# Performance work log

Measured on AMD Instinct MI355X. Metric: run time of the kernel, lower is better.

The kernel has to match this reference:

```python
import jax, jax.numpy as jnp
import numpy as np

B, N_SOURCES, H, W = 32, 262144, 256, 256


def setup_inputs() -> dict:
    key = jax.random.key(0)
    k1, k2, k3, k4 = jax.random.split(key, 4)
    return {
        "point_rates": jax.random.uniform(k1, (B, N_SOURCES), dtype=jnp.float32),
        "spatial": jax.random.uniform(k2, (B, 2, H, W), dtype=jnp.float32),
        "gia": jax.random.uniform(k3, (B, H, W), dtype=jnp.float32),
        "all_source_coords": jax.random.uniform(k4, (N_SOURCES, 2), dtype=jnp.float32),
    }


def reference(point_rates, spatial, gia, all_source_coords):
    # point_rates: [B, N], spatial: [B, 2, H, W], gia: [B, H, W], coords: [N, 2]
    _, _, h, w = spatial.shape
    sx = all_source_coords[:, 0]  # [N]
    sy = all_source_coords[:, 1]  # [N]

    def per_batch(pr, sp, g):
        # pr: [N], sp: [2, H, W], g: [H, W]
        xmin, xmax = sp[0].min(), sp[0].max()
        ymin, ymax = sp[1].min(), sp[1].max()
        in_view = ((sx >= xmin) & (sx <= xmax) & (sy >= ymin) & (sy <= ymax))
        nx = (sx - xmin) / (xmax - xmin)
        ny = (sy - ymin) / (ymax - ymin)
        px = jnp.clip(jnp.round(nx * (w - 1)).astype(jnp.int32), 0, w - 1)
        py = jnp.clip(jnp.round(ny * (h - 1)).astype(jnp.int32), 0, h - 1)
        # out-of-view sources contribute zero (instead of being gathered out)
        em = pr * g[py, px] * in_view.astype(pr.dtype)  # [N]
        field = jnp.zeros((h, w), dtype=pr.dtype).at[py, px].add(em)
        return field[None]  # [1, H, W]

    return jax.vmap(per_batch)(point_rates, spatial, gia)  # [B, 1, H, W]
```

## Files before the change

### kernel.cpp

```cpp
#include <hip/hip_runtime.h>
#include <math.h>

#define BATCH 32
#define NSRC  262144
#define HH    256
#define WW    256
#define HW    (HH * WW)
#define NBLK  16

#define ZBANDS 16
#define ZBAND_PIX (HW / ZBANDS)
#define ZCAP   18432
#define SPILL_CAP 131072
#define FIX_SCALE 524288.0f
#define FIX_INV   (1.0f / 524288.0f)
#define WS_ZCURS_OFF  8192
#define WS_ZSPCNT_OFF 10240
#define WS_ZSPILL_OFF 16384
#define WS_ZARENA_OFF (WS_ZSPILL_OFF + SPILL_CAP * 8)
#define WS_Z_BYTES    (WS_ZARENA_OFF + (size_t)BATCH * ZBANDS * ZCAP * 4)

#define FB_BANDS 8
#define FB_BAND_PIX (HW / FB_BANDS)

__global__ void box_kernel(const float* __restrict__ spatial,
                           float4* __restrict__ partials,
                           unsigned int* __restrict__ zero_tab,
                           int zero_n) {
    const int b   = blockIdx.y;
    const int blk = blockIdx.x;
    const int tid = threadIdx.x;

    if (zero_tab && blk == 0 && b == 0) {
        for (int j = tid; j < zero_n; j += 256) zero_tab[j] = 0u;
    }

    const int chunk = HW / NBLK;
    const float* xs = spatial + (size_t)b * 2 * HW + (size_t)blk * chunk;
    const float* ys = xs + HW;

    float xmn = 1e30f, xmx = -1e30f, ymn = 1e30f, ymx = -1e30f;
    const float4* xs4 = (const float4*)xs;
    const float4* ys4 = (const float4*)ys;
#pragma unroll
    for (int k = 0; k < 4; k++) {
        float4 vx = xs4[k * 256 + tid];
        float4 vy = ys4[k * 256 + tid];
        xmn = fminf(xmn, fminf(fminf(vx.x, vx.y), fminf(vx.z, vx.w)));
        xmx = fmaxf(xmx, fmaxf(fmaxf(vx.x, vx.y), fmaxf(vx.z, vx.w)));
        ymn = fminf(ymn, fminf(fminf(vy.x, vy.y), fminf(vy.z, vy.w)));
        ymx = fmaxf(ymx, fmaxf(fmaxf(vy.x, vy.y), fmaxf(vy.z, vy.w)));
    }
#pragma unroll
    for (int off = 32; off > 0; off >>= 1) {
        xmn = fminf(xmn, __shfl_down(xmn, off));
        xmx = fmaxf(xmx, __shfl_down(xmx, off));
        ymn = fminf(ymn, __shfl_down(ymn, off));
        ymx = fmaxf(ymx, __shfl_down(ymx, off));
    }
    __shared__ float4 s[4];
    if ((tid & 63) == 0) s[tid >> 6] = make_float4(xmn, xmx, ymn, ymx);
    __syncthreads();
    if (tid == 0) {
        float4 r = s[0];
#pragma unroll
        for (int wv = 1; wv < 4; wv++) {
            float4 t = s[wv];
            r.x = fminf(r.x, t.x); r.y = fmaxf(r.y, t.y);
            r.z = fminf(r.z, t.z); r.w = fmaxf(r.w, t.w);
        }
        partials[b * NBLK + blk] = r;
    }
}

__device__ __forceinline__ float4 fold_box(const float4* __restrict__ partials,
                                           int b, int tid, float4* sbox) {
    if (tid < 64) {
        float4 p = make_float4(1e30f, -1e30f, 1e30f, -1e30f);
        if (tid < NBLK) p = partials[b * NBLK + tid];
        float xmn = p.x, xmx = p.y, ymn = p.z, ymx = p.w;
#pragma unroll
        for (int off = 8; off > 0; off >>= 1) {
            xmn = fminf(xmn, __shfl_down(xmn, off));
            xmx = fmaxf(xmx, __shfl_down(xmx, off));
            ymn = fminf(ymn, __shfl_down(ymn, off));
            ymx = fmaxf(ymx, __shfl_down(ymx, off));
        }
        if (tid == 0) *sbox = make_float4(xmn, xmx, ymn, ymx);
    }
    __syncthreads();
    return *sbox;
}

__device__ __forceinline__ int route_of(float cx, float cy, float xmin,
                                        float ymin, float invx, float invy) {
    const float nx = __fmul_rn(__fsub_rn(cx, xmin), invx);
    const float ny = __fmul_rn(__fsub_rn(cy, ymin), invy);
    int px = (int)rintf(__fmul_rn(nx, 255.0f));
    int py = (int)rintf(__fmul_rn(ny, 255.0f));
    px = px < 0 ? 0 : (px > 255 ? 255 : px);
    py = py < 0 ? 0 : (py > 255 ? 255 : py);
    return py * WW + px;
}


__global__ __launch_bounds__(256) void scatter_lds_kernel(
    const float* __restrict__ point_rates, const float2* __restrict__ coords,
    const float4* __restrict__ partials, unsigned int* __restrict__ cursors,
    unsigned int* __restrict__ arena, unsigned int* __restrict__ spill_cnt,
    uint2* __restrict__ spill) {
    const int b   = blockIdx.y;
    const int tid = threadIdx.x;
    __shared__ float4 sbox;
    __shared__ unsigned int cnt[ZBANDS];
    __shared__ unsigned int gbase[ZBANDS];

    if (tid < ZBANDS) cnt[tid] = 0u;
    const float4 box = fold_box(partials, b, tid, &sbox);
    const float xmin = box.x, xmax = box.y, ymin = box.z, ymax = box.w;
    const float invx = __fdiv_rn(1.0f, __fsub_rn(xmax, xmin));
    const float invy = __fdiv_rn(1.0f, __fsub_rn(ymax, ymin));

    const float* prb = point_rates + (size_t)b * NSRC;
    const int base = blockIdx.x * 4096;

    unsigned int ent[16];
    unsigned int meta[16];

#pragma unroll
    for (int kk = 0; kk < 16; kk += 4) {
        float2 c0, c1, c2, c3;
        float  p0, p1, p2, p3;
        {
            const int i0 = base + (kk + 0) * 256 + tid;
            const int i1 = base + (kk + 1) * 256 + tid;
            const int i2 = base + (kk + 2) * 256 + tid;
            const int i3 = base + (kk + 3) * 256 + tid;
            c0 = coords[i0]; c1 = coords[i1];
            c2 = coords[i2]; c3 = coords[i3];
            p0 = prb[i0]; p1 = prb[i1]; p2 = prb[i2]; p3 = prb[i3];
        }
        asm volatile(""
                     : "+v"(c0.x), "+v"(c0.y), "+v"(p0),
                       "+v"(c1.x), "+v"(c1.y), "+v"(p1),
                       "+v"(c2.x), "+v"(c2.y), "+v"(p2),
                       "+v"(c3.x), "+v"(c3.y), "+v"(p3));
#define RANK_ONE(J, CC, PP)                                                  \
    {                                                                        \
        const bool valid = !(CC.x < xmin || CC.x > xmax ||                   \
                             CC.y < ymin || CC.y > ymax);                    \
        const int idx = route_of(CC.x, CC.y, xmin, ymin, invx, invy);        \
        const unsigned int fixed =                                           \
            (unsigned int)(__fmul_rn(PP, FIX_SCALE) + 0.5f);                 \
        ent[kk + J] =                                                        \
            (unsigned int)(idx & (ZBAND_PIX - 1)) | (fixed << 12);           \
        const int z = idx >> 12;                                             \
        unsigned int rank = 0u;                                              \
        if (valid) rank = atomicAdd(&cnt[z], 1u);                            \
        meta[kk + J] = valid                                                 \
            ? (((unsigned int)z << 16) | rank) : 0xFFFFFFFFu;                \
    }
        RANK_ONE(0, c0, p0)
        RANK_ONE(1, c1, p1)
        RANK_ONE(2, c2, p2)
        RANK_ONE(3, c3, p3)
#undef RANK_ONE
    }
    __syncthreads();

    if (tid < ZBANDS) {
        gbase[tid] = atomicAdd(&cursors[b * ZBANDS + tid], cnt[tid]);
    }
    __syncthreads();

    unsigned int* ab = arena + (size_t)b * ZBANDS * ZCAP;
#pragma unroll
    for (int k = 0; k < 16; k++) {
        const unsigned int mt = meta[k];
        if (mt == 0xFFFFFFFFu) continue;
        const unsigned int z = mt >> 16;
        const unsigned int slot = gbase[z] + (mt & 0xFFFFu);
        if (slot < ZCAP) {
            ab[(size_t)z * ZCAP + slot] = ent[k];
        } else {
            const unsigned int pos = atomicAdd(spill_cnt, 1u);
            if (pos < SPILL_CAP) {
                const unsigned int e = ent[k];
                const unsigned int pix =
                    (z << 12) | (e & (ZBAND_PIX - 1));
                const float pr = __fmul_rn((float)(e >> 12), FIX_INV);
                spill[pos] = make_uint2(((unsigned int)b << 16) | pix,
                                        __float_as_uint(pr));
            }
        }
    }
}

__global__ __launch_bounds__(1024) void accum_g_kernel(
    const unsigned int* __restrict__ arena, const float* __restrict__ gia,
    const unsigned int* __restrict__ cursors, float* __restrict__ out) {
    __shared__ unsigned int acc[ZBAND_PIX];
    const int z   = blockIdx.x;
    const int b   = blockIdx.y;
    const int tid = threadIdx.x;

    const unsigned int n_raw = cursors[b * ZBANDS + z];
    const float4* g4 =
        (const float4*)(gia + (size_t)b * HW + (size_t)z * ZBAND_PIX);
    float4 g = g4[tid];
    asm volatile("" : "+v"(g.x), "+v"(g.y), "+v"(g.z), "+v"(g.w));

    ((uint4*)acc)[tid] = make_uint4(0u, 0u, 0u, 0u);
    __syncthreads();

    unsigned int n = n_raw;
    if (n > ZCAP) n = ZCAP;
    const uint4* a4 = (const uint4*)(arena + ((size_t)b * ZBANDS + z) * ZCAP);

#define DO_E(w)                                                              \
    atomicAdd(&acc[(w) & (ZBAND_PIX - 1)], (w) >> 12);
    const unsigned int n4 = n >> 2;
    unsigned int j = tid;
    for (; j + 3u * 1024u < n4; j += 4u * 1024u) {
        uint4 e0 = a4[j];
        uint4 e1 = a4[j + 1024u];
        uint4 e2 = a4[j + 2048u];
        uint4 e3 = a4[j + 3072u];
        asm volatile(""
                     : "+v"(e0.x), "+v"(e0.y), "+v"(e0.z), "+v"(e0.w),
                       "+v"(e1.x), "+v"(e1.y), "+v"(e1.z), "+v"(e1.w),
                       "+v"(e2.x), "+v"(e2.y), "+v"(e2.z), "+v"(e2.w),
                       "+v"(e3.x), "+v"(e3.y), "+v"(e3.z), "+v"(e3.w));
        DO_E(e0.x) DO_E(e0.y) DO_E(e0.z) DO_E(e0.w)
        DO_E(e1.x) DO_E(e1.y) DO_E(e1.z) DO_E(e1.w)
        DO_E(e2.x) DO_E(e2.y) DO_E(e2.z) DO_E(e2.w)
        DO_E(e3.x) DO_E(e3.y) DO_E(e3.z) DO_E(e3.w)
    }
    for (; j < n4; j += 1024u) {
        const uint4 e = a4[j];
        DO_E(e.x) DO_E(e.y) DO_E(e.z) DO_E(e.w)
    }
    const unsigned int* a1 = (const unsigned int*)a4;
    for (unsigned int jj = (n4 << 2) + tid; jj < n; jj += 1024u) {
        const unsigned int w = a1[jj];
        DO_E(w)
    }
#undef DO_E
    __syncthreads();

    float4* o4 = (float4*)(out + (size_t)b * HW + (size_t)z * ZBAND_PIX);
    const uint4 a = ((const uint4*)acc)[tid];
    o4[tid] = make_float4(
        __fmul_rn(__fmul_rn((float)a.x, FIX_INV), g.x),
        __fmul_rn(__fmul_rn((float)a.y, FIX_INV), g.y),
        __fmul_rn(__fmul_rn((float)a.z, FIX_INV), g.z),
        __fmul_rn(__fmul_rn((float)a.w, FIX_INV), g.w));
}

__global__ void spill_kernel(const unsigned int* __restrict__ spill_cnt,
                             const uint2* __restrict__ spill,
                             const float* __restrict__ gia,
                             float* __restrict__ out) {
    unsigned int n = *spill_cnt;
    if (n > SPILL_CAP) n = SPILL_CAP;
    for (unsigned int j = blockIdx.x * 256 + threadIdx.x; j < n;
         j += gridDim.x * 256) {
        const uint2 e = spill[j];
        const unsigned int b = e.x >> 16;
        const unsigned int pix = e.x & 0xFFFFu;
        const float pr = __uint_as_float(e.y);
        atomicAdd(&out[(size_t)b * HW + pix],
                  __fmul_rn(pr, gia[(size_t)b * HW + pix]));
    }
}


__global__ __launch_bounds__(512) void accum_recompute_kernel(
    const float* __restrict__ point_rates, const float* __restrict__ gia,
    const float2* __restrict__ coords, const float4* __restrict__ partials,
    float* __restrict__ out) {
    __shared__ float acc[FB_BAND_PIX];
    __shared__ float4 sbox;
    const int z   = blockIdx.x;
    const int b   = blockIdx.y;
    const int tid = threadIdx.x;

    const float4 box = fold_box(partials, b, tid, &sbox);
    const float xmin = box.x, xmax = box.y, ymin = box.z, ymax = box.w;
    const float invx = __fdiv_rn(1.0f, __fsub_rn(xmax, xmin));
    const float invy = __fdiv_rn(1.0f, __fsub_rn(ymax, ymin));

    for (int j = tid; j < FB_BAND_PIX; j += 512) acc[j] = 0.f;
    __syncthreads();

    const float* prb = point_rates + (size_t)b * NSRC;
    const float* gb  = gia + (size_t)b * HW;
    const int lo = z * FB_BAND_PIX, hi = lo + FB_BAND_PIX;

    for (int i = tid; i < NSRC; i += 512) {
        const float2 c = coords[i];
        if (c.x < xmin || c.x > xmax || c.y < ymin || c.y > ymax) continue;
        const int idx = route_of(c.x, c.y, xmin, ymin, invx, invy);
        if (idx < lo || idx >= hi) continue;
        const float em = __fmul_rn(prb[i], gb[idx]);
        atomicAdd(&acc[idx - lo], em);
    }
    __syncthreads();

    float4* o4 = (float4*)(out + (size_t)b * HW + (size_t)z * FB_BAND_PIX);
    const float4* a4 = (const float4*)acc;
    for (int j = tid; j < FB_BAND_PIX / 4; j += 512) o4[j] = a4[j];
}

extern "C" void kernel_launch(void* const* d_in, const int* in_sizes, int n_in,
                              void* d_out, int out_size, void* d_ws, size_t ws_size,
                              hipStream_t stream) {
    const float* point_rates = (const float*)d_in[0];
    const float* spatial     = (const float*)d_in[1];
    const float* gia         = (const float*)d_in[2];
    const float2* coords     = (const float2*)d_in[3];
    float* out = (float*)d_out;

    char* ws = (char*)d_ws;
    float4* partials = (float4*)ws;

    if (ws_size >= WS_Z_BYTES) {
        unsigned int* cursors   = (unsigned int*)(ws + WS_ZCURS_OFF);
        unsigned int* spill_cnt = (unsigned int*)(ws + WS_ZSPCNT_OFF);
        uint2*        spill     = (uint2*)(ws + WS_ZSPILL_OFF);
        unsigned int* arena     = (unsigned int*)(ws + WS_ZARENA_OFF);

        box_kernel<<<dim3(NBLK, BATCH), 256, 0, stream>>>(
            spatial, partials, cursors, BATCH * ZBANDS + 1);
        scatter_lds_kernel<<<dim3(NSRC / 4096, BATCH), 256, 0, stream>>>(
            point_rates, coords, partials, cursors, arena, spill_cnt, spill);
        accum_g_kernel<<<dim3(ZBANDS, BATCH), 1024, 0, stream>>>(
            arena, gia, cursors, out);
        spill_kernel<<<4, 256, 0, stream>>>(spill_cnt, spill, gia, out);
    } else {
        box_kernel<<<dim3(NBLK, BATCH), 256, 0, stream>>>(
            spatial, partials, nullptr, 0);
        accum_recompute_kernel<<<dim3(FB_BANDS, BATCH), 512, 0, stream>>>(
            point_rates, gia, coords, partials, out);
    }
}
```

Baseline: 124.6 us.

## Replace global band cursors with per-block fixed-capacity segments in arena

The scatter kernel now writes each entry straight into a per-(batch, block, band) segment of fixed capacity, using the LDS rank, and records the per-segment counts in a table. This removes the global atomic cursor reservation, the second barrier and the register buffering of entries and metadata. The accumulate kernel then has each wavefront walk several of these segments. In exchange the arena grows, segment reads are shorter and less coalesced, and any band overflow beyond the per-segment cap falls back to the spill path.

```diff
diff --git a/kernel.cpp b/kernel.cpp
--- a/kernel.cpp
+++ b/kernel.cpp
@@ -10,15 +10,16 @@
 
 #define ZBANDS 16
 #define ZBAND_PIX (HW / ZBANDS)
-#define ZCAP   18432
+#define NB_SCAT 64
+#define CAP_PB  400
 #define SPILL_CAP 131072
 #define FIX_SCALE 524288.0f
 #define FIX_INV   (1.0f / 524288.0f)
-#define WS_ZCURS_OFF  8192
-#define WS_ZSPCNT_OFF 10240
-#define WS_ZSPILL_OFF 16384
-#define WS_ZARENA_OFF (WS_ZSPILL_OFF + SPILL_CAP * 8)
-#define WS_Z_BYTES    (WS_ZARENA_OFF + (size_t)BATCH * ZBANDS * ZCAP * 4)
+#define WS_SPCNT_OFF  8192
+#define WS_CNTTAB_OFF 16384
+#define WS_SPILL_OFF  (WS_CNTTAB_OFF + BATCH * NB_SCAT * ZBANDS * 4)
+#define WS_ARENA_OFF  (WS_SPILL_OFF + SPILL_CAP * 8)
+#define WS_BYTES      (WS_ARENA_OFF + (size_t)BATCH * NB_SCAT * ZBANDS * CAP_PB * 4)
 
 #define FB_BANDS 8
 #define FB_BAND_PIX (HW / FB_BANDS)
@@ -103,17 +104,16 @@
     return py * WW + px;
 }
 
-
-__global__ __launch_bounds__(256) void scatter_lds_kernel(
+__global__ __launch_bounds__(256) void scatter_seg_kernel(
     const float* __restrict__ point_rates, const float2* __restrict__ coords,
-    const float4* __restrict__ partials, unsigned int* __restrict__ cursors,
-    unsigned int* __restrict__ arena, unsigned int* __restrict__ spill_cnt,
+    const float4* __restrict__ partials, unsigned int* __restrict__ arena,
+    unsigned int* __restrict__ cnt_tab, unsigned int* __restrict__ spill_cnt,
     uint2* __restrict__ spill) {
     const int b   = blockIdx.y;
+    const int blk = blockIdx.x;
     const int tid = threadIdx.x;
     __shared__ float4 sbox;
     __shared__ unsigned int cnt[ZBANDS];
-    __shared__ unsigned int gbase[ZBANDS];
 
     if (tid < ZBANDS) cnt[tid] = 0u;
     const float4 box = fold_box(partials, b, tid, &sbox);
@@ -122,10 +122,9 @@
     const float invy = __fdiv_rn(1.0f, __fsub_rn(ymax, ymin));
 
     const float* prb = point_rates + (size_t)b * NSRC;
-    const int base = blockIdx.x * 4096;
-
-    unsigned int ent[16];
-    unsigned int meta[16];
+    const int base = blk * 4096;
+    unsigned int* seg =
+        arena + ((size_t)b * NB_SCAT + blk) * ZBANDS * CAP_PB;
 
 #pragma unroll
     for (int kk = 0; kk < 16; kk += 4) {
@@ -145,66 +144,58 @@
                        "+v"(c1.x), "+v"(c1.y), "+v"(p1),
                        "+v"(c2.x), "+v"(c2.y), "+v"(p2),
                        "+v"(c3.x), "+v"(c3.y), "+v"(p3));
-#define RANK_ONE(J, CC, PP)                                                  \
+#define DO_ONE(CC, PP)                                                       \
     {                                                                        \
         const bool valid = !(CC.x < xmin || CC.x > xmax ||                   \
                              CC.y < ymin || CC.y > ymax);                    \
         const int idx = route_of(CC.x, CC.y, xmin, ymin, invx, invy);        \
         const unsigned int fixed =                                           \
             (unsigned int)(__fmul_rn(PP, FIX_SCALE) + 0.5f);                 \
-        ent[kk + J] =                                                        \
+        const unsigned int e =                                               \
             (unsigned int)(idx & (ZBAND_PIX - 1)) | (fixed << 12);           \
         const int z = idx >> 12;                                             \
-        unsigned int rank = 0u;                                              \
-        if (valid) rank = atomicAdd(&cnt[z], 1u);                            \
-        meta[kk + J] = valid                                                 \
-            ? (((unsigned int)z << 16) | rank) : 0xFFFFFFFFu;                \
-    }
-        RANK_ONE(0, c0, p0)
-        RANK_ONE(1, c1, p1)
-        RANK_ONE(2, c2, p2)
-        RANK_ONE(3, c3, p3)
-#undef RANK_ONE
+        if (valid) {                                                         \
+            const unsigned int rank = atomicAdd(&cnt[z], 1u);                \
+            if (rank < CAP_PB) {                                             \
+                seg[(unsigned int)z * CAP_PB + rank] = e;                    \
+            } else {                                                         \
+                const unsigned int pos = atomicAdd(spill_cnt, 1u);           \
+                if (pos < SPILL_CAP) {                                       \
+                    const unsigned int pix =                                 \
+                        ((unsigned int)z << 12) | (e & (ZBAND_PIX - 1));     \
+                    const float prq = __fmul_rn((float)(e >> 12), FIX_INV);  \
+                    spill[pos] = make_uint2(                                 \
+                        ((unsigned int)b << 16) | pix,                       \
+                        __float_as_uint(prq));                               \
+                }                                                            \
+            }                                                                \
+        }                                                                    \
+    }
+        DO_ONE(c0, p0)
+        DO_ONE(c1, p1)
+        DO_ONE(c2, p2)
+        DO_ONE(c3, p3)
+#undef DO_ONE
     }
     __syncthreads();
 
     if (tid < ZBANDS) {
-        gbase[tid] = atomicAdd(&cursors[b * ZBANDS + tid], cnt[tid]);
-    }
-    __syncthreads();
-
-    unsigned int* ab = arena + (size_t)b * ZBANDS * ZCAP;
-#pragma unroll
-    for (int k = 0; k < 16; k++) {
-        const unsigned int mt = meta[k];
-        if (mt == 0xFFFFFFFFu) continue;
-        const unsigned int z = mt >> 16;
-        const unsigned int slot = gbase[z] + (mt & 0xFFFFu);
-        if (slot < ZCAP) {
-            ab[(size_t)z * ZCAP + slot] = ent[k];
-        } else {
-            const unsigned int pos = atomicAdd(spill_cnt, 1u);
-            if (pos < SPILL_CAP) {
-                const unsigned int e = ent[k];
-                const unsigned int pix =
-                    (z << 12) | (e & (ZBAND_PIX - 1));
-                const float pr = __fmul_rn((float)(e >> 12), FIX_INV);
-                spill[pos] = make_uint2(((unsigned int)b << 16) | pix,
-                                        __float_as_uint(pr));
-            }
-        }
+        unsigned int c = cnt[tid];
+        cnt_tab[((size_t)b * NB_SCAT + blk) * ZBANDS + tid] =
+            c < CAP_PB ? c : CAP_PB;
     }
 }
 
 __global__ __launch_bounds__(1024) void accum_g_kernel(
     const unsigned int* __restrict__ arena, const float* __restrict__ gia,
-    const unsigned int* __restrict__ cursors, float* __restrict__ out) {
+    const unsigned int* __restrict__ cnt_tab, float* __restrict__ out) {
     __shared__ unsigned int acc[ZBAND_PIX];
-    const int z   = blockIdx.x;
-    const int b   = blockIdx.y;
-    const int tid = threadIdx.x;
-
-    const unsigned int n_raw = cursors[b * ZBANDS + z];
+    const int z    = blockIdx.x;
+    const int b    = blockIdx.y;
+    const int tid  = threadIdx.x;
+    const int wave = tid >> 6;
+    const int lane = tid & 63;
+
     const float4* g4 =
         (const float4*)(gia + (size_t)b * HW + (size_t)z * ZBAND_PIX);
     float4 g = g4[tid];
@@ -213,37 +204,24 @@
     ((uint4*)acc)[tid] = make_uint4(0u, 0u, 0u, 0u);
     __syncthreads();
 
-    unsigned int n = n_raw;
-    if (n > ZCAP) n = ZCAP;
-    const uint4* a4 = (const uint4*)(arena + ((size_t)b * ZBANDS + z) * ZCAP);
-
 #define DO_E(w)                                                              \
     atomicAdd(&acc[(w) & (ZBAND_PIX - 1)], (w) >> 12);
-    const unsigned int n4 = n >> 2;
-    unsigned int j = tid;
-    for (; j + 3u * 1024u < n4; j += 4u * 1024u) {
-        uint4 e0 = a4[j];
-        uint4 e1 = a4[j + 1024u];
-        uint4 e2 = a4[j + 2048u];
-        uint4 e3 = a4[j + 3072u];
-        asm volatile(""
-                     : "+v"(e0.x), "+v"(e0.y), "+v"(e0.z), "+v"(e0.w),
-                       "+v"(e1.x), "+v"(e1.y), "+v"(e1.z), "+v"(e1.w),
-                       "+v"(e2.x), "+v"(e2.y), "+v"(e2.z), "+v"(e2.w),
-                       "+v"(e3.x), "+v"(e3.y), "+v"(e3.z), "+v"(e3.w));
-        DO_E(e0.x) DO_E(e0.y) DO_E(e0.z) DO_E(e0.w)
-        DO_E(e1.x) DO_E(e1.y) DO_E(e1.z) DO_E(e1.w)
-        DO_E(e2.x) DO_E(e2.y) DO_E(e2.z) DO_E(e2.w)
-        DO_E(e3.x) DO_E(e3.y) DO_E(e3.z) DO_E(e3.w)
-    }
-    for (; j < n4; j += 1024u) {
-        const uint4 e = a4[j];
-        DO_E(e.x) DO_E(e.y) DO_E(e.z) DO_E(e.w)
-    }
-    const unsigned int* a1 = (const unsigned int*)a4;
-    for (unsigned int jj = (n4 << 2) + tid; jj < n; jj += 1024u) {
-        const unsigned int w = a1[jj];
-        DO_E(w)
+#pragma unroll
+    for (int s = 0; s < NB_SCAT / 16; s++) {
+        const int blk = wave + s * 16;
+        const unsigned int n =
+            cnt_tab[((size_t)b * NB_SCAT + blk) * ZBANDS + z];
+        const unsigned int* seg =
+            arena + (((size_t)b * NB_SCAT + blk) * ZBANDS + (unsigned)z) *
+                        CAP_PB;
+        const unsigned int n4 = n >> 2;
+        for (unsigned int j = lane; j < n4; j += 64u) {
+            const uint4 e = ((const uint4*)seg)[j];
+            DO_E(e.x) DO_E(e.y) DO_E(e.z) DO_E(e.w)
+        }
+        for (unsigned int j = (n4 << 2) + lane; j < n; j += 64u) {
+            DO_E(seg[j])
+        }
     }
 #undef DO_E
     __syncthreads();
@@ -324,18 +302,18 @@
     char* ws = (char*)d_ws;
     float4* partials = (float4*)ws;
 
-    if (ws_size >= WS_Z_BYTES) {
-        unsigned int* cursors   = (unsigned int*)(ws + WS_ZCURS_OFF);
-        unsigned int* spill_cnt = (unsigned int*)(ws + WS_ZSPCNT_OFF);
-        uint2*        spill     = (uint2*)(ws + WS_ZSPILL_OFF);
-        unsigned int* arena     = (unsigned int*)(ws + WS_ZARENA_OFF);
+    if (ws_size >= WS_BYTES) {
+        unsigned int* spill_cnt = (unsigned int*)(ws + WS_SPCNT_OFF);
+        unsigned int* cnt_tab   = (unsigned int*)(ws + WS_CNTTAB_OFF);
+        uint2*        spill     = (uint2*)(ws + WS_SPILL_OFF);
+        unsigned int* arena     = (unsigned int*)(ws + WS_ARENA_OFF);
 
         box_kernel<<<dim3(NBLK, BATCH), 256, 0, stream>>>(
-            spatial, partials, cursors, BATCH * ZBANDS + 1);
-        scatter_lds_kernel<<<dim3(NSRC / 4096, BATCH), 256, 0, stream>>>(
-            point_rates, coords, partials, cursors, arena, spill_cnt, spill);
+            spatial, partials, spill_cnt, 1);
+        scatter_seg_kernel<<<dim3(NB_SCAT, BATCH), 256, 0, stream>>>(
+            point_rates, coords, partials, arena, cnt_tab, spill_cnt, spill);
         accum_g_kernel<<<dim3(ZBANDS, BATCH), 1024, 0, stream>>>(
-            arena, gia, cursors, out);
+            arena, gia, cnt_tab, out);
         spill_kernel<<<4, 256, 0, stream>>>(spill_cnt, spill, gia, out);
     } else {
         box_kernel<<<dim3(NBLK, BATCH), 256, 0, stream>>>(
```

Result: slower. 134.4 us (+7.8%).
